# Optimization experiments

Measured on AMD Instinct MI355X. Metric: run time of the kernel, lower is better.

Reference implementation:

```python
import jax, jax.numpy as jnp
import numpy as np

N = 20000   # nodes
D = 64      # emb_dim
H = 512     # 8 * emb_dim
E = 320000  # edges per graph


def setup_inputs() -> dict:
    key = jax.random.key(0)
    ks = jax.random.split(key, 40)
    i = iter(range(40))
    def nrm(shape, s=0.05):
        return jax.random.normal(ks[next(i)], shape, dtype=jnp.float32) * s
    def edges():
        return jax.random.randint(ks[next(i)], (E,), 0, N, dtype=jnp.int32)
    inp = {}
    inp['k_emb'] = nrm((N, D), 1.0)
    inp['pr_src'] = edges(); inp['pr_dst'] = edges()
    inp['pr_ew'] = jax.random.uniform(ks[next(i)], (E,), dtype=jnp.float32)
    inp['cc_src'] = edges(); inp['cc_dst'] = edges()
    inp['cc_ew'] = jax.random.uniform(ks[next(i)], (E,), dtype=jnp.float32)
    inp['sps_src'] = edges(); inp['sps_dst'] = edges()
    inp['pr_Ws0'] = nrm((D, H)); inp['pr_Wn0'] = nrm((D, H)); inp['pr_b0'] = jnp.zeros((H,), jnp.float32)
    inp['pr_Ws1'] = nrm((H, D)); inp['pr_Wn1'] = nrm((H, D)); inp['pr_b1'] = jnp.zeros((D,), jnp.float32)
    inp['cc_Ws0'] = nrm((D, H)); inp['cc_Wn0'] = nrm((D, H)); inp['cc_b0'] = jnp.zeros((H,), jnp.float32)
    inp['cc_Ws1'] = nrm((H, D)); inp['cc_Wn1'] = nrm((H, D)); inp['cc_b1'] = jnp.zeros((D,), jnp.float32)
    inp['ap_Ws0'] = nrm((D, D)); inp['ap_Wn0'] = nrm((D, D)); inp['ap_b0'] = jnp.zeros((D,), jnp.float32)
    inp['ap_Ws1'] = nrm((D, D)); inp['ap_Wn1'] = nrm((D, D)); inp['ap_b1'] = jnp.zeros((D,), jnp.float32)
    inp['att_W'] = nrm((D, D)); inp['att_b'] = jnp.zeros((D,), jnp.float32)
    return inp


def _sage(x, src, dst, ew, Ws, Wn, b):
    # DGL SAGEConv 'mean': neigh = sum(w_e * h_src) / in_degree; out = x@Ws + neigh@Wn + b
    msg = x[src]                                  # [E, din] gather
    if ew is not None:
        msg = msg * ew[:, None]
    agg = jax.ops.segment_sum(msg, dst, num_segments=N)            # [N, din]
    deg = jax.ops.segment_sum(jnp.ones((msg.shape[0],), x.dtype), dst, num_segments=N)
    agg = agg / jnp.maximum(deg, 1.0)[:, None]
    return x @ Ws + agg @ Wn + b


def reference(k_emb, pr_src, pr_dst, pr_ew, cc_src, cc_dst, cc_ew, sps_src, sps_dst,
              pr_Ws0, pr_Wn0, pr_b0, pr_Ws1, pr_Wn1, pr_b1,
              cc_Ws0, cc_Wn0, cc_b0, cc_Ws1, cc_Wn1, cc_b1,
              ap_Ws0, ap_Wn0, ap_b0, ap_Ws1, ap_Wn1, ap_b1,
              att_W, att_b):
    pr = jax.nn.relu(_sage(k_emb, pr_src, pr_dst, pr_ew, pr_Ws0, pr_Wn0, pr_b0))
    pr = _sage(pr, pr_src, pr_dst, pr_ew, pr_Ws1, pr_Wn1, pr_b1)            # [N, D]
    cc = jax.nn.relu(_sage(k_emb, cc_src, cc_dst, cc_ew, cc_Ws0, cc_Wn0, cc_b0))
    cc = _sage(cc, cc_src, cc_dst, cc_ew, cc_Ws1, cc_Wn1, cc_b1)            # [N, D]
    ap = jax.nn.relu(_sage(k_emb, sps_src, sps_dst, None, ap_Ws0, ap_Wn0, ap_b0))
    ap = _sage(ap, sps_src, sps_dst, None, ap_Ws1, ap_Wn1, ap_b1)           # [N, D]
    # APATT fusion
    z = jnp.stack((pr, cc), axis=1)                      # [N, 2, D]
    proj = jnp.tanh(z @ att_W + att_b)                   # [N, 2, D]
    w = jnp.sum(ap[:, None, :] * proj, axis=-1, keepdims=True).mean(0)  # [2, 1]
    beta = jax.nn.softmax(w, axis=0)                     # [2, 1]
    return (beta * z).sum(axis=1)                        # [N, D]
```

## Files before the change

### kernel.cpp

```cpp
#include <hip/hip_runtime.h>
#include <hip/hip_fp16.h>

#define NN 20000
#define NP 20032
#define DD 64
#define HH 512
#define EE 320000
#define ATT_BLOCKS 625
#define BLOCKS_E (EE / 256)
#define CB 157
#define EPB 4096
#define B1_BLOCKS ((EE + EPB - 1) / EPB)
#define ZERO_N (3 * NN + 3 * CB)
#define ZERO_BLOCKS ((ZERO_N + 255) / 256)

typedef __attribute__((ext_vector_type(8))) short short8;
typedef __attribute__((ext_vector_type(4))) float f32x4;

__device__ __forceinline__ ushort f2bf(float f) {
    union { float f; unsigned u; } v; v.f = f;
    unsigned r = v.u + 0x7FFF + ((v.u >> 16) & 1);
    return (ushort)(r >> 16);
}
__device__ __forceinline__ float bf2f(ushort h) {
    union { unsigned u; float f; } v; v.u = ((unsigned)h) << 16;
    return v.f;
}
__device__ __forceinline__ float ew_of(uint w) {
    __half h = __ushort_as_half((ushort)(w >> 16));
    return __half2float(h);
}

__global__ __launch_bounds__(256) void hist3(const int* __restrict__ d0,
                                             const int* __restrict__ d1,
                                             const int* __restrict__ d2,
                                             int* __restrict__ cnt) {
    int g = blockIdx.x / BLOCKS_E;
    int e = (blockIdx.x % BLOCKS_E) * 256 + threadIdx.x;
    const int* d = (g == 0) ? d0 : (g == 1) ? d1 : d2;
    if (e < EE) atomicAdd(&cnt[g * NN + d[e]], 1);
}

__global__ __launch_bounds__(1024) void scan_kernel(const int* __restrict__ cnt,
                                                    int* __restrict__ rowptr,
                                                    float* __restrict__ invd) {
    __shared__ int part[1024];
    int g = blockIdx.x;
    const int* c = cnt + g * NN;
    int* rp = rowptr + g * (NN + 1);
    int tid = threadIdx.x;
    const int CH = (NN + 1023) / 1024;
    int i0 = tid * CH;
    int s = 0;
    for (int i = 0; i < CH; ++i) { int idx = i0 + i; if (idx < NN) s += c[idx]; }
    part[tid] = s;
    __syncthreads();
    for (int off = 1; off < 1024; off <<= 1) {
        int v = (tid >= off) ? part[tid - off] : 0;
        __syncthreads();
        part[tid] += v;
        __syncthreads();
    }
    int run = (tid > 0) ? part[tid - 1] : 0;
    for (int i = 0; i < CH; ++i) {
        int idx = i0 + i;
        if (idx < NN) {
            int cv = c[idx];
            rp[idx] = run; run += cv;
            invd[g * NN + idx] = 1.0f / fmaxf((float)cv, 1.0f);
        }
    }
    if (tid == 1023) rp[NN] = part[1023];
}

__global__ __launch_bounds__(256) void bucket_coarse(
    const int* __restrict__ s0, const int* __restrict__ d0, const float* __restrict__ w0,
    const int* __restrict__ s1, const int* __restrict__ d1, const float* __restrict__ w1,
    const int* __restrict__ s2, const int* __restrict__ d2,
    const int* __restrict__ rowptr,
    int* __restrict__ ccur,
    uint* __restrict__ ce,
    ushort* __restrict__ cd) {
    __shared__ int cnt_s[CB];
    __shared__ int off_s[CB];
    __shared__ int pos_s[CB];
    __shared__ int gbase[CB];
    __shared__ uint lword[EPB];
    __shared__ ushort ldst[EPB];
    int g = blockIdx.x / B1_BLOCKS;
    int blk = blockIdx.x % B1_BLOCKS;
    const int* S = (g == 0) ? s0 : (g == 1) ? s1 : s2;
    const int* D = (g == 0) ? d0 : (g == 1) ? d1 : d2;
    const float* W = (g == 0) ? w0 : (g == 1) ? w1 : nullptr;
    int e0 = blk * EPB;
    int n = min(EPB, EE - e0);
    for (int i = threadIdx.x; i < CB; i += 256) cnt_s[i] = 0;
    __syncthreads();
    for (int i = threadIdx.x; i < n; i += 256)
        atomicAdd(&cnt_s[D[e0 + i] >> 7], 1);
    __syncthreads();
    if (threadIdx.x == 0) {
        int run = 0;
        for (int i = 0; i < CB; ++i) { off_s[i] = run; run += cnt_s[i]; }
    }
    __syncthreads();
    if (threadIdx.x < CB) pos_s[threadIdx.x] = off_s[threadIdx.x];
    __syncthreads();
    for (int i = threadIdx.x; i < n; i += 256) {
        int e = e0 + i;
        int d = D[e];
        int p = atomicAdd(&pos_s[d >> 7], 1);
        ushort ewh = (g < 2) ? __half_as_ushort(__float2half(W[e])) : 0;
        lword[p] = ((uint)ewh << 16) | (uint)(S[e] & 0xFFFF);
        ldst[p] = (ushort)d;
    }
    __syncthreads();
    if (threadIdx.x < CB)
        gbase[threadIdx.x] = atomicAdd(&ccur[g * CB + threadIdx.x], cnt_s[threadIdx.x]);
    __syncthreads();
    const int* rp = rowptr + g * (NN + 1);
    for (int j = threadIdx.x; j < n; j += 256) {
        ushort d = ldst[j];
        int cb = d >> 7;
        int gpos = rp[cb << 7] + gbase[cb] + (j - off_s[cb]);
        ce[(size_t)g * EE + gpos] = lword[j];
        cd[(size_t)g * EE + gpos] = d;
    }
}

__global__ __launch_bounds__(256) void bucket_fine(
    const int* __restrict__ rowptr,
    const uint* __restrict__ ce, const ushort* __restrict__ cd,
    uint* __restrict__ edge_s,
    ushort* __restrict__ src_s2) {
    __shared__ int rp_s[129];
    __shared__ int cur_s[128];
    int g = blockIdx.x / CB;
    int cb = blockIdx.x % CB;
    const int* rp = rowptr + g * (NN + 1);
    int n0 = cb << 7;
    int n1 = min(n0 + 128, NN);
    int m = n1 - n0;
    if (threadIdx.x <= m) rp_s[threadIdx.x] = rp[n0 + threadIdx.x];
    if (threadIdx.x < m) cur_s[threadIdx.x] = 0;
    __syncthreads();
    int beg = rp_s[0], end = rp_s[m];
    for (int j = beg + threadIdx.x; j < end; j += 256) {
        uint e = ce[(size_t)g * EE + j];
        int dl = (int)cd[(size_t)g * EE + j] - n0;
        int pos = rp_s[dl] + atomicAdd(&cur_s[dl], 1);
        if (g < 2) edge_s[(size_t)g * EE + pos] = e;
        else src_s2[pos] = (ushort)(e & 0xFFFF);
    }
}

__global__ __launch_bounds__(256) void pull_cast3(const ushort* __restrict__ xh,
                                                  const int* __restrict__ rowptr,
                                                  const uint* __restrict__ edge_s,
                                                  const ushort* __restrict__ src_s2,
                                                  const float* __restrict__ invd,
                                                  ushort* __restrict__ aggh) {
    __shared__ float part[2][64];
    int gwave = (blockIdx.x * 256 + threadIdx.x) >> 6;
    int lane = threadIdx.x & 63;
    int wv = threadIdx.x >> 6;
    int pairIdx = wv >> 1;
    int sub = wv & 1;
    int node = gwave >> 1;
    if (node >= 3 * NN) return;
    int g = node / NN, n = node % NN;
    const int* rp = rowptr + g * (NN + 1);
    int beg = rp[n], end = rp[n + 1];
    int mid = (beg + end + 1) >> 1;
    int lo = sub ? mid : beg;
    int hi = sub ? end : mid;
    float a[4] = {};
    int i = lo;
    if (g < 2) {
        const uint* es = edge_s + (size_t)g * EE;
        for (; i + 4 <= hi; i += 4) {
#pragma unroll
            for (int j = 0; j < 4; ++j) {
                uint e = es[i + j];
                a[j] = fmaf(bf2f(xh[(e & 0xFFFF) * DD + lane]), ew_of(e), a[j]);
            }
        }
        for (; i < hi; ++i) {
            uint e = es[i];
            a[0] = fmaf(bf2f(xh[(e & 0xFFFF) * DD + lane]), ew_of(e), a[0]);
        }
    } else {
        for (; i + 4 <= hi; i += 4) {
#pragma unroll
            for (int j = 0; j < 4; ++j)
                a[j] += bf2f(xh[(int)src_s2[i + j] * DD + lane]);
        }
        for (; i < hi; ++i) a[0] += bf2f(xh[(int)src_s2[i] * DD + lane]);
    }
    float acc = (a[0] + a[1]) + (a[2] + a[3]);
    if (sub == 1) part[pairIdx][lane] = acc;
    __syncthreads();
    if (sub == 0) {
        acc += part[pairIdx][lane];
        aggh[((size_t)g * NP + n) * 64 + lane] = f2bf(acc * invd[g * NN + n]);
    }
}

__global__ __launch_bounds__(256) void pull_combine3(const ushort* __restrict__ xnh,
                                                     const int* __restrict__ rowptr,
                                                     const uint* __restrict__ edge_s,
                                                     const ushort* __restrict__ src_s2,
                                                     const float* __restrict__ invd,
                                                     const float* __restrict__ b_pr,
                                                     const float* __restrict__ b_cc,
                                                     const float* __restrict__ b_ap,
                                                     float* __restrict__ o_pr,
                                                     float* __restrict__ o_cc,
                                                     float* __restrict__ o_ap) {
    __shared__ float part[2][64];
    int gwave = (blockIdx.x * 256 + threadIdx.x) >> 6;
    int lane = threadIdx.x & 63;
    int wv = threadIdx.x >> 6;
    int pairIdx = wv >> 1;
    int sub = wv & 1;
    int node = gwave >> 1;
    if (node >= 3 * NN) return;
    int g = node / NN, n = node % NN;
    const int* rp = rowptr + g * (NN + 1);
    const ushort* x = xnh + (size_t)g * NP * 64;
    int beg = rp[n], end = rp[n + 1];
    int mid = (beg + end + 1) >> 1;
    int lo = sub ? mid : beg;
    int hi = sub ? end : mid;
    float a[4] = {};
    int i = lo;
    if (g < 2) {
        const uint* es = edge_s + (size_t)g * EE;
        for (; i + 4 <= hi; i += 4) {
#pragma unroll
            for (int j = 0; j < 4; ++j) {
                uint e = es[i + j];
                a[j] = fmaf(bf2f(x[(e & 0xFFFF) * DD + lane]), ew_of(e), a[j]);
            }
        }
        for (; i < hi; ++i) {
            uint e = es[i];
            a[0] = fmaf(bf2f(x[(e & 0xFFFF) * DD + lane]), ew_of(e), a[0]);
        }
    } else {
        for (; i + 4 <= hi; i += 4) {
#pragma unroll
            for (int j = 0; j < 4; ++j)
                a[j] += bf2f(x[(int)src_s2[i + j] * DD + lane]);
        }
        for (; i < hi; ++i) a[0] += bf2f(x[(int)src_s2[i] * DD + lane]);
    }
    float acc = (a[0] + a[1]) + (a[2] + a[3]);
    if (sub == 1) part[pairIdx][lane] = acc;
    __syncthreads();
    if (sub == 0) {
        acc += part[pairIdx][lane];
        const float* bias = (g == 0) ? b_pr : (g == 1) ? b_cc : b_ap;
        float* out = (g == 0) ? o_pr : (g == 1) ? o_cc : o_ap;
        out[n * DD + lane] += acc * invd[g * NN + n] + bias[lane];
    }
}

__global__ __launch_bounds__(256) void pack_all(
    const float* __restrict__ pr_Ws0, const float* __restrict__ pr_Wn0,
    const float* __restrict__ cc_Ws0, const float* __restrict__ cc_Wn0,
    const float* __restrict__ pr_Ws1, const float* __restrict__ pr_Wn1,
    const float* __restrict__ cc_Ws1, const float* __restrict__ cc_Wn1,
    const float* __restrict__ ap_Ws0, const float* __restrict__ ap_Wn0,
    const float* __restrict__ ap_Ws1, const float* __restrict__ ap_Wn1,
    const float* __restrict__ k_emb,
    ushort* __restrict__ W0h_pr, ushort* __restrict__ W0h_cc,
    ushort* __restrict__ W1h_pr, ushort* __restrict__ W1h_cc,
    ushort* __restrict__ W0h_ap, ushort* __restrict__ W1h_ap,
    ushort* __restrict__ xh,
    int* __restrict__ zero_base) {
    int b = blockIdx.x;
    int tid = threadIdx.x;
    if (b < 512) {
        int t = (b & 255) * 256 + tid;
        const float* Ws = (b < 256) ? pr_Ws0 : cc_Ws0;
        const float* Wn = (b < 256) ? pr_Wn0 : cc_Wn0;
        ushort* o = (b < 256) ? W0h_pr : W0h_cc;
        int c = t >> 7, k = t & 127;
        o[t] = f2bf((k < 64) ? Ws[k * 512 + c] : Wn[(k - 64) * 512 + c]);
    } else if (b < 1024) {
        int t = ((b - 512) & 255) * 256 + tid;
        const float* Ws = (b < 768) ? pr_Ws1 : cc_Ws1;
        const float* Wn = (b < 768) ? pr_Wn1 : cc_Wn1;
        ushort* o = (b < 768) ? W1h_pr : W1h_cc;
        int c = t >> 9, k = t & 511;
        o[t] = f2bf((c < 64) ? Ws[k * 64 + c] : Wn[k * 64 + (c - 64)]);
    } else if (b < 1056) {
        int t = (b - 1024) * 256 + tid;
        int c = t >> 7, k = t & 127;
        W0h_ap[t] = f2bf((k < 64) ? ap_Ws0[k * 64 + c] : ap_Wn0[(k - 64) * 64 + c]);
    } else if (b < 1088) {
        int t = (b - 1056) * 256 + tid;
        int c = t >> 6, k = t & 63;
        W1h_ap[t] = f2bf((c < 64) ? ap_Ws1[k * 64 + c] : ap_Wn1[k * 64 + (c - 64)]);
    } else if (b < 1088 + ZERO_BLOCKS) {
        int t = (b - 1088) * 256 + tid;
        if (t < ZERO_N) zero_base[t] = 0;
    } else {
        int t = (b - 1088 - ZERO_BLOCKS) * 256 + tid;
        if (t < NN * DD) xh[t] = f2bf(k_emb[t]);
    }
}

__global__ __launch_bounds__(512, 4) void fused_sage4(
    const ushort* __restrict__ xh,
    const ushort* __restrict__ aggA,
    const ushort* __restrict__ W0a, const ushort* __restrict__ W1a,
    const ushort* __restrict__ W0b, const ushort* __restrict__ W1b,
    const float* __restrict__ b0a, const float* __restrict__ b0b,
    float* __restrict__ outS0, float* __restrict__ outS1,
    ushort* __restrict__ xnh, int nblk) {
    constexpr int LROW = 136;
    __shared__ ushort Ahs[64 * LROW];
    __shared__ ushort h1s[64 * LROW];
    int br = blockIdx.x / nblk;
    int rb = blockIdx.x % nblk;
    const ushort* W0 = br ? W0b : W0a;
    const ushort* W1 = br ? W1b : W1a;
    const float* b0 = br ? b0b : b0a;
    float* outS = br ? outS1 : outS0;
    ushort* outX = xnh + (size_t)br * NP * 64;
    const ushort* agg = aggA + (size_t)br * NP * 64;
    int row0 = rb * 64;

    int wv = threadIdx.x >> 6;
    int lane = threadIdx.x & 63;
    int lrow = lane & 15;
    int koff = (lane >> 4) * 8;
    int crow = (lane >> 4) * 4;

    {
        int r = threadIdx.x >> 3;
        int seg = threadIdx.x & 7;
        const ushort* src = (seg < 4) ? (xh + (size_t)(row0 + r) * 64 + seg * 16)
                                      : (agg + (size_t)(row0 + r) * 64 + (seg - 4) * 16);
        *(short8*)&Ahs[r * LROW + seg * 16] = *(const short8*)src;
        *(short8*)&Ahs[r * LROW + seg * 16 + 8] = *(const short8*)(src + 8);
    }
    __syncthreads();

    f32x4 C[4] = {};
#pragma unroll
    for (int p = 0; p < 4; ++p) {
        {
            short8 B[4];
#pragma unroll
            for (int kk = 0; kk < 4; ++kk)
                B[kk] = *(const short8*)(W0 + (size_t)(p * 128 + wv * 16 + lrow) * 128 + kk * 32 + koff);
            f32x4 acc[4] = {};
#pragma unroll
            for (int rg = 0; rg < 4; ++rg) {
#pragma unroll
                for (int kk = 0; kk < 4; ++kk) {
                    short8 a = *(const short8*)&Ahs[(rg * 16 + lrow) * LROW + kk * 32 + koff];
                    acc[rg] = __builtin_amdgcn_mfma_f32_16x16x32_bf16(a, B[kk], acc[rg], 0, 0, 0);
                }
            }
            float bb = b0[p * 128 + wv * 16 + lrow];
#pragma unroll
            for (int rg = 0; rg < 4; ++rg) {
#pragma unroll
                for (int r = 0; r < 4; ++r) {
                    float v = fmaxf(acc[rg][r] + bb, 0.0f);
                    h1s[(rg * 16 + crow + r) * LROW + wv * 16 + lrow] = f2bf(v);
                }
            }
        }
        __syncthreads();
        {
            short8 B[4];
#pragma unroll
            for (int kc = 0; kc < 4; ++kc)
                B[kc] = *(const short8*)(W1 + (size_t)(wv * 16 + lrow) * HH + p * 128 + kc * 32 + koff);
#pragma unroll
            for (int rg = 0; rg < 4; ++rg) {
#pragma unroll
                for (int kc = 0; kc < 4; ++kc) {
                    short8 a = *(const short8*)&h1s[(rg * 16 + lrow) * LROW + kc * 32 + koff];
                    C[rg] = __builtin_amdgcn_mfma_f32_16x16x32_bf16(a, B[kc], C[rg], 0, 0, 0);
                }
            }
        }
        __syncthreads();
    }
    int col = wv * 16 + lrow;
    if (col < 64) {
        float* o = outS + col;
#pragma unroll
        for (int rg = 0; rg < 4; ++rg)
#pragma unroll
            for (int r = 0; r < 4; ++r) {
                int row = row0 + rg * 16 + crow + r;
                if (row < NN) o[(size_t)row * 64] = C[rg][r];
            }
    } else {
        ushort* o = outX + (col - 64);
#pragma unroll
        for (int rg = 0; rg < 4; ++rg)
#pragma unroll
            for (int r = 0; r < 4; ++r) {
                int row = row0 + rg * 16 + crow + r;
                if (row < NN) o[(size_t)row * 64] = f2bf(C[rg][r]);
            }
    }
}

__global__ __launch_bounds__(256, 4) void fused_sage_ap(
    const ushort* __restrict__ xh,
    const ushort* __restrict__ agg,
    const ushort* __restrict__ W0,
    const ushort* __restrict__ W1,
    const float* __restrict__ b0,
    float* __restrict__ outS,
    ushort* __restrict__ outX) {
    constexpr int LROW = 72;
    __shared__ ushort h1s[16 * LROW];
    int wv = threadIdx.x >> 6;
    int lane = threadIdx.x & 63;
    int lrow = lane & 15;
    int koff = (lane >> 4) * 8;
    int crow = (lane >> 4) * 4;
    int row0 = blockIdx.x * 16;

    {
        const size_t aoff = (size_t)(row0 + lrow) * 64 + koff;
        short8 aF[4];
#pragma unroll
        for (int kk = 0; kk < 2; ++kk) {
            aF[kk]     = *(const short8*)(xh + aoff + kk * 32);
            aF[2 + kk] = *(const short8*)(agg + aoff + kk * 32);
        }
        f32x4 acc = {};
#pragma unroll
        for (int kk = 0; kk < 4; ++kk) {
            short8 b = *(const short8*)(W0 + (size_t)(wv * 16 + lrow) * 128 + kk * 32 + koff);
            acc = __builtin_amdgcn_mfma_f32_16x16x32_bf16(aF[kk], b, acc, 0, 0, 0);
        }
        float bb = b0[wv * 16 + lrow];
#pragma unroll
        for (int r = 0; r < 4; ++r) {
            h1s[(crow + r) * LROW + wv * 16 + lrow] = f2bf(fmaxf(acc[r] + bb, 0.0f));
        }
    }
    __syncthreads();
    {
        f32x4 C2[2] = {};
#pragma unroll
        for (int kc = 0; kc < 2; ++kc) {
            short8 a = *(const short8*)&h1s[lrow * LROW + kc * 32 + koff];
#pragma unroll
            for (int c = 0; c < 2; ++c) {
                short8 b = *(const short8*)(W1 + (size_t)(wv * 32 + c * 16 + lrow) * 64 + kc * 32 + koff);
                C2[c] = __builtin_amdgcn_mfma_f32_16x16x32_bf16(a, b, C2[c], 0, 0, 0);
            }
        }
#pragma unroll
        for (int c = 0; c < 2; ++c) {
            int col = wv * 32 + c * 16 + lrow;
#pragma unroll
            for (int r = 0; r < 4; ++r) {
                int row = row0 + crow + r;
                if (row < NN) {
                    if (col < 64) outS[(size_t)row * 64 + col] = C2[c][r];
                    else outX[(size_t)row * 64 + (col - 64)] = f2bf(C2[c][r]);
                }
            }
        }
    }
}

__global__ __launch_bounds__(256) void att_stage1(const float* __restrict__ pr,
                                                  const float* __restrict__ cc,
                                                  const float* __restrict__ ap,
                                                  const float* __restrict__ attW,
                                                  const float* __restrict__ attb,
                                                  float2* __restrict__ partial) {
    __shared__ float red[8];
    int lane = threadIdx.x & 63;
    int wv = threadIdx.x >> 6;
    int gw = blockIdx.x * 4 + wv;
    const int nwaves = ATT_BLOCKS * 4;
    float b = attb[lane];
    float c0 = 0.f, c1 = 0.f;
    for (int n = gw; n < NN; n += nwaves) {
        float p0 = 0.f, p1 = 0.f;
        for (int k = 0; k < DD; ++k) {
            float w = attW[k * DD + lane];
            p0 = fmaf(pr[n * DD + k], w, p0);
            p1 = fmaf(cc[n * DD + k], w, p1);
        }
        float a = ap[n * DD + lane];
        c0 += a * tanhf(p0 + b);
        c1 += a * tanhf(p1 + b);
    }
#pragma unroll
    for (int off = 32; off; off >>= 1) {
        c0 += __shfl_xor(c0, off);
        c1 += __shfl_xor(c1, off);
    }
    if (lane == 0) { red[wv * 2] = c0; red[wv * 2 + 1] = c1; }
    __syncthreads();
    if (threadIdx.x == 0) {
        partial[blockIdx.x] = make_float2(red[0] + red[2] + red[4] + red[6],
                                          red[1] + red[3] + red[5] + red[7]);
    }
}

__global__ __launch_bounds__(64) void att_stage2(const float2* __restrict__ partial,
                                                 float* __restrict__ w_acc) {
    int lane = threadIdx.x;
    float s0 = 0.f, s1 = 0.f;
    for (int i = lane; i < ATT_BLOCKS; i += 64) {
        float2 p = partial[i];
        s0 += p.x; s1 += p.y;
    }
#pragma unroll
    for (int off = 32; off; off >>= 1) {
        s0 += __shfl_xor(s0, off);
        s1 += __shfl_xor(s1, off);
    }
    if (lane == 0) { w_acc[0] = s0; w_acc[1] = s1; }
}

__global__ __launch_bounds__(256) void final_kernel(float* __restrict__ pr_out,
                                                    const float* __restrict__ cc,
                                                    const float* __restrict__ w_acc) {
    int t = blockIdx.x * blockDim.x + threadIdx.x;
    if (t >= NN * DD) return;
    float w0 = w_acc[0] * (1.0f / NN);
    float w1 = w_acc[1] * (1.0f / NN);
    float m = fmaxf(w0, w1);
    float e0 = __expf(w0 - m), e1 = __expf(w1 - m);
    float inv = 1.0f / (e0 + e1);
    pr_out[t] = (e0 * pr_out[t] + e1 * cc[t]) * inv;
}

extern "C" void kernel_launch(void* const* d_in, const int* in_sizes, int n_in,
                              void* d_out, int out_size, void* d_ws, size_t ws_size,
                              hipStream_t stream) {
    const float* k_emb  = (const float*)d_in[0];
    const int*   pr_src = (const int*)d_in[1];
    const int*   pr_dst = (const int*)d_in[2];
    const float* pr_ew  = (const float*)d_in[3];
    const int*   cc_src = (const int*)d_in[4];
    const int*   cc_dst = (const int*)d_in[5];
    const float* cc_ew  = (const float*)d_in[6];
    const int*   sps_src = (const int*)d_in[7];
    const int*   sps_dst = (const int*)d_in[8];
    const float* pr_Ws0 = (const float*)d_in[9];
    const float* pr_Wn0 = (const float*)d_in[10];
    const float* pr_b0  = (const float*)d_in[11];
    const float* pr_Ws1 = (const float*)d_in[12];
    const float* pr_Wn1 = (const float*)d_in[13];
    const float* pr_b1  = (const float*)d_in[14];
    const float* cc_Ws0 = (const float*)d_in[15];
    const float* cc_Wn0 = (const float*)d_in[16];
    const float* cc_b0  = (const float*)d_in[17];
    const float* cc_Ws1 = (const float*)d_in[18];
    const float* cc_Wn1 = (const float*)d_in[19];
    const float* cc_b1  = (const float*)d_in[20];
    const float* ap_Ws0 = (const float*)d_in[21];
    const float* ap_Wn0 = (const float*)d_in[22];
    const float* ap_b0  = (const float*)d_in[23];
    const float* ap_Ws1 = (const float*)d_in[24];
    const float* ap_Wn1 = (const float*)d_in[25];
    const float* ap_b1  = (const float*)d_in[26];
    const float* att_W  = (const float*)d_in[27];
    const float* att_b  = (const float*)d_in[28];
    float* out = (float*)d_out;

    char* base = (char*)d_ws;
    size_t off = 0;
    auto alloc = [&](size_t bytes) -> void* {
        void* p = base + off;
        off = (off + bytes + 255) & ~(size_t)255;
        return p;
    };
    float*  invd   = (float*)alloc((size_t)3 * NN * 4);
    int*    cnt    = (int*)alloc((size_t)ZERO_N * 4);
    int*    ccur   = cnt + 3 * NN;
    int*    rowptr = (int*)alloc((size_t)3 * (NN + 1) * 4);
    uint*   edge_s = (uint*)alloc((size_t)2 * EE * 4);
    ushort* src_s2 = (ushort*)alloc((size_t)EE * 2);
    uint*   ce     = (uint*)alloc((size_t)3 * EE * 4);
    ushort* cd     = (ushort*)alloc((size_t)3 * EE * 2);
    float*  w_acc  = (float*)alloc(64);
    float2* att_partial = (float2*)alloc(ATT_BLOCKS * 8);
    ushort* xnh    = (ushort*)alloc((size_t)3 * NP * DD * 2);
    float*  out_cc = (float*)alloc((size_t)NN * DD * 4);
    float*  out_ap = (float*)alloc((size_t)NN * DD * 4);
    ushort* xh     = (ushort*)alloc((size_t)NP * DD * 2);
    ushort* aggh   = (ushort*)alloc((size_t)3 * NP * DD * 2);
    ushort* W0h_pr = (ushort*)alloc(512 * 128 * 2);
    ushort* W0h_cc = (ushort*)alloc(512 * 128 * 2);
    ushort* W0h_ap = (ushort*)alloc(64 * 128 * 2);
    ushort* W1h_pr = (ushort*)alloc(128 * 512 * 2);
    ushort* W1h_cc = (ushort*)alloc(128 * 512 * 2);
    ushort* W1h_ap = (ushort*)alloc(128 * 64 * 2);
    float*  out_pr = out;

    const int TB = 256;
    const int blocks_ND = (NN * DD) / TB;
    const int blocks_pull = (3 * NN * 2 * 64) / TB;
    const int NBLK64 = NP / 64;

    pack_all<<<1088 + ZERO_BLOCKS + blocks_ND, TB, 0, stream>>>(
        pr_Ws0, pr_Wn0, cc_Ws0, cc_Wn0, pr_Ws1, pr_Wn1, cc_Ws1, cc_Wn1,
        ap_Ws0, ap_Wn0, ap_Ws1, ap_Wn1, k_emb,
        W0h_pr, W0h_cc, W1h_pr, W1h_cc, W0h_ap, W1h_ap, xh, cnt);

    hist3<<<3 * BLOCKS_E, TB, 0, stream>>>(pr_dst, cc_dst, sps_dst, cnt);
    scan_kernel<<<3, 1024, 0, stream>>>(cnt, rowptr, invd);
    bucket_coarse<<<3 * B1_BLOCKS, TB, 0, stream>>>(pr_src, pr_dst, pr_ew,
                                                    cc_src, cc_dst, cc_ew,
                                                    sps_src, sps_dst,
                                                    rowptr, ccur, ce, cd);
    bucket_fine<<<3 * CB, TB, 0, stream>>>(rowptr, ce, cd, edge_s, src_s2);

    pull_cast3<<<blocks_pull, TB, 0, stream>>>(xh, rowptr, edge_s, src_s2, invd, aggh);

    fused_sage4<<<2 * NBLK64, 512, 0, stream>>>(
        xh, aggh,
        W0h_pr, W1h_pr, W0h_cc, W1h_cc,
        pr_b0, cc_b0, out_pr, out_cc, xnh, NBLK64);
    fused_sage_ap<<<NP / 16, 256, 0, stream>>>(
        xh, aggh + (size_t)2 * NP * 64,
        W0h_ap, W1h_ap, ap_b0, out_ap, xnh + (size_t)2 * NP * 64);

    pull_combine3<<<blocks_pull, TB, 0, stream>>>(xnh, rowptr, edge_s, src_s2, invd,
                                                  pr_b1, cc_b1, ap_b1,
                                                  out_pr, out_cc, out_ap);

    att_stage1<<<ATT_BLOCKS, TB, 0, stream>>>(out_pr, out_cc, out_ap, att_W, att_b, att_partial);
    att_stage2<<<1, 64, 0, stream>>>(att_partial, w_acc);
    final_kernel<<<blocks_ND, TB, 0, stream>>>(out_pr, out_cc, w_acc);
}
```

Before: 300.4 us.

## Restructure pull aggregation to one wave per node with 4 edges in flight

The two pull kernels change from two waves per node (each lane owning one feature, with the halves merged through shared memory and a block barrier) to one wave per node. Each 16-lane quarter handles a different edge and each lane loads 4 bf16 features as a ushort4, followed by a cross-quarter shuffle reduction. This removes the LDS exchange and __syncthreads, halves the wave count, and widens the gathered loads. In exchange each node's edges are walked serially by a single wave, so there is less parallelism per node.

```diff
diff --git a/kernel.cpp b/kernel.cpp
--- a/kernel.cpp
+++ b/kernel.cpp
@@ -160,49 +160,41 @@
                                                   const ushort* __restrict__ src_s2,
                                                   const float* __restrict__ invd,
                                                   ushort* __restrict__ aggh) {
-    __shared__ float part[2][64];
-    int gwave = (blockIdx.x * 256 + threadIdx.x) >> 6;
+    int wid = (blockIdx.x * 256 + threadIdx.x) >> 6;
     int lane = threadIdx.x & 63;
-    int wv = threadIdx.x >> 6;
-    int pairIdx = wv >> 1;
-    int sub = wv & 1;
-    int node = gwave >> 1;
-    if (node >= 3 * NN) return;
-    int g = node / NN, n = node % NN;
+    if (wid >= 3 * NN) return;
+    int g = wid / NN, n = wid % NN;
     const int* rp = rowptr + g * (NN + 1);
     int beg = rp[n], end = rp[n + 1];
-    int mid = (beg + end + 1) >> 1;
-    int lo = sub ? mid : beg;
-    int hi = sub ? end : mid;
-    float a[4] = {};
-    int i = lo;
-    if (g < 2) {
-        const uint* es = edge_s + (size_t)g * EE;
-        for (; i + 4 <= hi; i += 4) {
-#pragma unroll
-            for (int j = 0; j < 4; ++j) {
-                uint e = es[i + j];
-                a[j] = fmaf(bf2f(xh[(e & 0xFFFF) * DD + lane]), ew_of(e), a[j]);
-            }
-        }
-        for (; i < hi; ++i) {
-            uint e = es[i];
-            a[0] = fmaf(bf2f(xh[(e & 0xFFFF) * DD + lane]), ew_of(e), a[0]);
-        }
-    } else {
-        for (; i + 4 <= hi; i += 4) {
-#pragma unroll
-            for (int j = 0; j < 4; ++j)
-                a[j] += bf2f(xh[(int)src_s2[i + j] * DD + lane]);
-        }
-        for (; i < hi; ++i) a[0] += bf2f(xh[(int)src_s2[i] * DD + lane]);
-    }
-    float acc = (a[0] + a[1]) + (a[2] + a[3]);
-    if (sub == 1) part[pairIdx][lane] = acc;
-    __syncthreads();
-    if (sub == 0) {
-        acc += part[pairIdx][lane];
-        aggh[((size_t)g * NP + n) * 64 + lane] = f2bf(acc * invd[g * NN + n]);
+    int q = lane >> 4, fl = lane & 15;
+    float a0 = 0.f, a1 = 0.f, a2 = 0.f, a3 = 0.f;
+    for (int i = beg; i < end; i += 4) {
+        int e = i + q;
+        bool valid = e < end;
+        int s; float w;
+        if (g < 2) {
+            uint ew = valid ? edge_s[(size_t)g * EE + e] : 0u;
+            s = (int)(ew & 0xFFFF);
+            w = valid ? ew_of(ew) : 0.f;
+        } else {
+            s = valid ? (int)src_s2[e] : 0;
+            w = valid ? 1.f : 0.f;
+        }
+        ushort4 v = *(const ushort4*)(xh + (size_t)s * DD + fl * 4);
+        a0 = fmaf(bf2f(v.x), w, a0);
+        a1 = fmaf(bf2f(v.y), w, a1);
+        a2 = fmaf(bf2f(v.z), w, a2);
+        a3 = fmaf(bf2f(v.w), w, a3);
+    }
+    a0 += __shfl_xor(a0, 16); a0 += __shfl_xor(a0, 32);
+    a1 += __shfl_xor(a1, 16); a1 += __shfl_xor(a1, 32);
+    a2 += __shfl_xor(a2, 16); a2 += __shfl_xor(a2, 32);
+    a3 += __shfl_xor(a3, 16); a3 += __shfl_xor(a3, 32);
+    if (q == 0) {
+        float sc = invd[g * NN + n];
+        ushort4 o;
+        o.x = f2bf(a0 * sc); o.y = f2bf(a1 * sc); o.z = f2bf(a2 * sc); o.w = f2bf(a3 * sc);
+        *(ushort4*)(aggh + ((size_t)g * NP + n) * 64 + fl * 4) = o;
     }
 }
 
@@ -217,52 +209,48 @@
                                                      float* __restrict__ o_pr,
                                                      float* __restrict__ o_cc,
                                                      float* __restrict__ o_ap) {
-    __shared__ float part[2][64];
-    int gwave = (blockIdx.x * 256 + threadIdx.x) >> 6;
+    int wid = (blockIdx.x * 256 + threadIdx.x) >> 6;
     int lane = threadIdx.x & 63;
-    int wv = threadIdx.x >> 6;
-    int pairIdx = wv >> 1;
-    int sub = wv & 1;
-    int node = gwave >> 1;
-    if (node >= 3 * NN) return;
-    int g = node / NN, n = node % NN;
+    if (wid >= 3 * NN) return;
+    int g = wid / NN, n = wid % NN;
     const int* rp = rowptr + g * (NN + 1);
     const ushort* x = xnh + (size_t)g * NP * 64;
     int beg = rp[n], end = rp[n + 1];
-    int mid = (beg + end + 1) >> 1;
-    int lo = sub ? mid : beg;
-    int hi = sub ? end : mid;
-    float a[4] = {};
-    int i = lo;
-    if (g < 2) {
-        const uint* es = edge_s + (size_t)g * EE;
-        for (; i + 4 <= hi; i += 4) {
-#pragma unroll
-            for (int j = 0; j < 4; ++j) {
-                uint e = es[i + j];
-                a[j] = fmaf(bf2f(x[(e & 0xFFFF) * DD + lane]), ew_of(e), a[j]);
-            }
-        }
-        for (; i < hi; ++i) {
-            uint e = es[i];
-            a[0] = fmaf(bf2f(x[(e & 0xFFFF) * DD + lane]), ew_of(e), a[0]);
-        }
-    } else {
-        for (; i + 4 <= hi; i += 4) {
-#pragma unroll
-            for (int j = 0; j < 4; ++j)
-                a[j] += bf2f(x[(int)src_s2[i + j] * DD + lane]);
-        }
-        for (; i < hi; ++i) a[0] += bf2f(x[(int)src_s2[i] * DD + lane]);
-    }
-    float acc = (a[0] + a[1]) + (a[2] + a[3]);
-    if (sub == 1) part[pairIdx][lane] = acc;
-    __syncthreads();
-    if (sub == 0) {
-        acc += part[pairIdx][lane];
+    int q = lane >> 4, fl = lane & 15;
+    float a0 = 0.f, a1 = 0.f, a2 = 0.f, a3 = 0.f;
+    for (int i = beg; i < end; i += 4) {
+        int e = i + q;
+        bool valid = e < end;
+        int s; float w;
+        if (g < 2) {
+            uint ew = valid ? edge_s[(size_t)g * EE + e] : 0u;
+            s = (int)(ew & 0xFFFF);
+            w = valid ? ew_of(ew) : 0.f;
+        } else {
+            s = valid ? (int)src_s2[e] : 0;
+            w = valid ? 1.f : 0.f;
+        }
+        ushort4 v = *(const ushort4*)(x + (size_t)s * DD + fl * 4);
+        a0 = fmaf(bf2f(v.x), w, a0);
+        a1 = fmaf(bf2f(v.y), w, a1);
+        a2 = fmaf(bf2f(v.z), w, a2);
+        a3 = fmaf(bf2f(v.w), w, a3);
+    }
+    a0 += __shfl_xor(a0, 16); a0 += __shfl_xor(a0, 32);
+    a1 += __shfl_xor(a1, 16); a1 += __shfl_xor(a1, 32);
+    a2 += __shfl_xor(a2, 16); a2 += __shfl_xor(a2, 32);
+    a3 += __shfl_xor(a3, 16); a3 += __shfl_xor(a3, 32);
+    if (q == 0) {
+        float sc = invd[g * NN + n];
         const float* bias = (g == 0) ? b_pr : (g == 1) ? b_cc : b_ap;
         float* out = (g == 0) ? o_pr : (g == 1) ? o_cc : o_ap;
-        out[n * DD + lane] += acc * invd[g * NN + n] + bias[lane];
+        float4 ov = *(float4*)(out + (size_t)n * DD + fl * 4);
+        float4 bv = *(const float4*)(bias + fl * 4);
+        ov.x += a0 * sc + bv.x;
+        ov.y += a1 * sc + bv.y;
+        ov.z += a2 * sc + bv.z;
+        ov.w += a3 * sc + bv.w;
+        *(float4*)(out + (size_t)n * DD + fl * 4) = ov;
     }
 }
 
@@ -611,7 +599,7 @@
 
     const int TB = 256;
     const int blocks_ND = (NN * DD) / TB;
-    const int blocks_pull = (3 * NN * 2 * 64) / TB;
+    const int blocks_pull = (3 * NN * 64) / TB;
     const int NBLK64 = NP / 64;
 
     pack_all<<<1088 + ZERO_BLOCKS + blocks_ND, TB, 0, stream>>>(
```

Result: faster. 272.8 us (-9.2%).
